# Performance work log

Hardware: AMD Instinct MI355X
Metric: run time of the kernel (lower is better)

## Reference

```python
import jax, jax.numpy as jnp
import numpy as np

HEADS = 8
DIM_HEAD = 64

def setup_inputs() -> dict:
    key = jax.random.key(0)
    ks = jax.random.split(key, 9)
    B, N1, N2, D = 4, 2048, 2048, 1024
    inner = HEADS * DIM_HEAD  # 512
    s_in = 1.0 / np.sqrt(D)
    s_inner = 1.0 / np.sqrt(inner)
    return {
        "x1": jax.random.normal(ks[0], (B, N1, D), jnp.float32),
        "x2": jax.random.normal(ks[1], (B, N2, D), jnp.float32),
        "Wq1": jax.random.normal(ks[2], (D, inner), jnp.float32) * s_in,
        "Wk1": jax.random.normal(ks[3], (D, inner), jnp.float32) * s_in,
        "Wv1": jax.random.normal(ks[4], (D, inner), jnp.float32) * s_in,
        "Wk2": jax.random.normal(ks[5], (D, inner), jnp.float32) * s_in,
        "Wv2": jax.random.normal(ks[6], (D, inner), jnp.float32) * s_in,
        "Wo": jax.random.normal(ks[7], (inner, D), jnp.float32) * s_inner,
        "bo": jnp.zeros((D,), jnp.float32),
    }

def reference(x1, x2, Wq1, Wk1, Wv1, Wk2, Wv2, Wo, bo):
    h, d = HEADS, DIM_HEAD
    scale = d ** (-0.5)
    B, N1, _ = x1.shape
    N2 = x2.shape[1]

    def split_heads(t, n):
        return t.reshape(B, n, h, d)  # [B, n, h, d]

    q1 = split_heads(x1 @ Wq1, N1)
    k1 = split_heads(x1 @ Wk1, N1)
    v1 = split_heads(x1 @ Wv1, N1)
    k2 = split_heads(x2 @ Wk2, N2)
    v2 = split_heads(x2 @ Wv2, N2)

    k = jnp.concatenate([k1, k2], axis=1)  # [B, N1+N2, h, d]
    v = jnp.concatenate([v1, v2], axis=1)

    # fp32 precision for QK^T (matches _ATTN_PRECISION == 'fp32')
    sim = jnp.einsum('bihd,bjhd->bhij', q1.astype(jnp.float32),
                     k.astype(jnp.float32)) * scale  # [B, h, N1, N1+N2]
    attn = jax.nn.softmax(sim, axis=-1)
    out = jnp.einsum('bhij,bjhd->bihd', attn, v)  # [B, N1, h, d]
    out = out.reshape(B, N1, h * d)
    return out @ Wo + bo
```

## Files before the change

kernel.cpp:

```cpp
#include <hip/hip_runtime.h>
#include <stdint.h>

typedef __bf16 bf16x8 __attribute__((ext_vector_type(8)));
typedef float f32x4 __attribute__((ext_vector_type(4)));
typedef unsigned short ushort_t;

#define MFMA16(a,b,c) __builtin_amdgcn_mfma_f32_16x16x32_bf16((a),(b),(c),0,0,0)

__device__ __forceinline__ unsigned short f2bf(float f){
    unsigned u = __builtin_bit_cast(unsigned, f);
    u += 0x7fffu + ((u>>16)&1u);
    return (unsigned short)(u>>16);
}
__device__ __forceinline__ unsigned pack2bf(float lo, float hi){
    unsigned a = __builtin_bit_cast(unsigned, lo) + 0x8000u;
    unsigned b = __builtin_bit_cast(unsigned, hi) + 0x8000u;
    return __builtin_amdgcn_perm(b, a, 0x07060302u);
}
__device__ __forceinline__ float fexp2(float x){
#if __has_builtin(__builtin_amdgcn_exp2f)
    return __builtin_amdgcn_exp2f(x);
#else
    return exp2f(x);
#endif
}

__device__ __forceinline__ void async16(ushort_t* lds, const ushort_t* g){
#if __has_builtin(__builtin_amdgcn_global_load_lds)
    __builtin_amdgcn_global_load_lds(
        (const __attribute__((address_space(1))) void*)g,
        (__attribute__((address_space(3))) void*)lds, 16, 0, 0);
#else
    const int l = (int)(threadIdx.x & 63u);
    *(uint4*)(lds + (size_t)l*8) = *(const uint4*)g;
#endif
}

__global__ __launch_bounds__(256) void convert_x(const float* __restrict__ src,
                                                 ushort_t* __restrict__ dst){
    size_t i = ((size_t)blockIdx.x*256 + threadIdx.x)*8;
    float4 a = *(const float4*)(src + i);
    float4 b = *(const float4*)(src + i + 4);
    uint4 o;
    o.x = pack2bf(a.x, a.y); o.y = pack2bf(a.z, a.w);
    o.z = pack2bf(b.x, b.y); o.w = pack2bf(b.z, b.w);
    *(uint4*)(dst + i) = o;
}

__global__ __launch_bounds__(256) void transpose_w(
    const float* __restrict__ w0, const float* __restrict__ w1,
    const float* __restrict__ w2, const float* __restrict__ w3,
    const float* __restrict__ w4,
    ushort_t* __restrict__ Wt1, ushort_t* __restrict__ Wt2)
{
    int z = blockIdx.z;
    const float* src; ushort_t* dst;
    if (z < 3)  { src = (z==0)?w0:((z==1)?w1:w2); dst = Wt1 + (size_t)z*512*1024; }
    else        { src = (z==3)?w3:w4;             dst = Wt2 + (size_t)(z-3)*512*1024; }
    const int K = 1024, N = 512;
    int k0 = blockIdx.x*32, n0 = blockIdx.y*32;
    __shared__ float T[32][33];
    int t = threadIdx.x;
    int kr = t>>3, nc = (t&7)*4;
    float4 v = *(const float4*)(src + (size_t)(k0+kr)*N + n0 + nc);
    T[kr][nc] = v.x; T[kr][nc+1] = v.y; T[kr][nc+2] = v.z; T[kr][nc+3] = v.w;
    __syncthreads();
    int nr = t>>3, kc = (t&7)*4;
    uint2 o;
    o.x = pack2bf(T[kc][nr],   T[kc+1][nr]);
    o.y = pack2bf(T[kc+2][nr], T[kc+3][nr]);
    *(uint2*)(dst + (size_t)(n0+nr)*K + k0 + kc) = o;
    (void)K;
}

__global__ __launch_bounds__(256) void transpose_wo(
    const float* __restrict__ src, ushort_t* __restrict__ dst)
{
    __shared__ float T[64][33];
    const int k0 = blockIdx.x*64;
    const int n0 = blockIdx.y*32;
    const int t = threadIdx.x;
    const int kr = t>>3, nc = (t&7)*4;
#pragma unroll
    for (int hf = 0; hf < 2; ++hf){
        float4 v = *(const float4*)(src + (size_t)(k0 + hf*32 + kr)*1024 + n0 + nc);
        T[hf*32+kr][nc]   = v.x; T[hf*32+kr][nc+1] = v.y;
        T[hf*32+kr][nc+2] = v.z; T[hf*32+kr][nc+3] = v.w;
    }
    __syncthreads();
    const int nr = t>>3, kc = (t&7)*8;
    ushort_t tmp[8];
#pragma unroll
    for (int e = 0; e < 8; ++e){
        int dp = kc + e;
        int d  = ((dp&3)<<4) | (dp>>2);
        tmp[e] = f2bf(T[d][nr]);
    }
    *(uint4*)(dst + (size_t)(n0+nr)*512 + k0 + kc) = *(uint4*)tmp;
}

template<int KD, int MODE>
__global__ __launch_bounds__(256) void gemm_bt(
    const ushort_t* __restrict__ A, const ushort_t* __restrict__ Bt,
    ushort_t* __restrict__ Qp, ushort_t* __restrict__ Kp, ushort_t* __restrict__ Vtp,
    float* __restrict__ outF, const float* __restrict__ bias, int koff)
{
    __shared__ ushort_t As[2][128][32];
    __shared__ ushort_t Bs[2][128][32];
    const int t = threadIdx.x;
    const int m0 = blockIdx.x*128, n0 = blockIdx.y*128;
    const int w = t>>6, l = t&63;
    const int quad = l>>4, lc = l&15;
    const int wr = (w>>1)*64, wc = (w&1)*64;

    f32x4 acc[4][4] = {};

    const int crow = l>>2;
    const int kseg = (l&3)*8;
    const ushort_t* gA0 = A  + (size_t)(m0 + w*32      + crow)*KD + kseg;
    const ushort_t* gA1 = A  + (size_t)(m0 + w*32 + 16 + crow)*KD + kseg;
    const ushort_t* gB0 = Bt + (size_t)(n0 + w*32      + crow)*KD + kseg;
    const ushort_t* gB1 = Bt + (size_t)(n0 + w*32 + 16 + crow)*KD + kseg;

    const int NK = KD/32;

    async16(&As[0][w*32][0],    gA0);
    async16(&As[0][w*32+16][0], gA1);
    async16(&Bs[0][w*32][0],    gB0);
    async16(&Bs[0][w*32+16][0], gB1);
    __syncthreads();

    for (int kk = 0; kk < NK; ++kk) {
        const int cur = kk & 1;
        if (kk + 1 < NK) {
            const int k0 = (kk+1)*32;
            const int nx = cur ^ 1;
            async16(&As[nx][w*32][0],    gA0 + k0);
            async16(&As[nx][w*32+16][0], gA1 + k0);
            async16(&Bs[nx][w*32][0],    gB0 + k0);
            async16(&Bs[nx][w*32+16][0], gB1 + k0);
        }
        bf16x8 af[4], bfv[4];
#pragma unroll
        for (int i = 0; i < 4; ++i) {
            af[i]  = *(const bf16x8*)&As[cur][wr + i*16 + lc][quad*8];
            bfv[i] = *(const bf16x8*)&Bs[cur][wc + i*16 + lc][quad*8];
        }
#pragma unroll
        for (int mt = 0; mt < 4; ++mt)
#pragma unroll
            for (int nt = 0; nt < 4; ++nt)
                acc[mt][nt] = MFMA16(af[mt], bfv[nt], acc[mt][nt]);
        __syncthreads();
    }

    if (MODE == 2) {
        float bv[4];
#pragma unroll
        for (int nt = 0; nt < 4; ++nt) bv[nt] = bias[n0 + wc + nt*16 + lc];
#pragma unroll
        for (int mt = 0; mt < 4; ++mt) {
            const int row = m0 + wr + mt*16 + quad*4;
#pragma unroll
            for (int nt = 0; nt < 4; ++nt) {
                const int col = n0 + wc + nt*16 + lc;
#pragma unroll
                for (int r = 0; r < 4; ++r)
                    outF[(size_t)(row+r)*1024 + col] = acc[mt][nt][r] + bv[nt];
            }
        }
    } else {
        const int sub = (MODE == 0) ? (n0>>9) : (1 + (n0>>9));
        const int hh  = ((n0 + wc)>>6) & 7;
        const int dp  = 4*lc;
        const float QSC = 0.18033688011112042f;
        if (sub == 0) {
#pragma unroll
            for (int mt = 0; mt < 4; ++mt) {
                const int row = m0 + wr + mt*16 + quad*4;
                const int b = row>>11, i = row & 2047;
#pragma unroll
                for (int r = 0; r < 4; ++r) {
                    uint2 o;
                    o.x = pack2bf(acc[mt][0][r]*QSC, acc[mt][1][r]*QSC);
                    o.y = pack2bf(acc[mt][2][r]*QSC, acc[mt][3][r]*QSC);
                    *(uint2*)(Qp + ((size_t)(b*8+hh)*2048 + i + r)*64 + dp) = o;
                }
            }
        } else if (sub == 1) {
#pragma unroll
            for (int mt = 0; mt < 4; ++mt) {
                const int row = m0 + wr + mt*16 + quad*4;
                const int b = row>>11, i = row & 2047;
#pragma unroll
                for (int r = 0; r < 4; ++r) {
                    uint2 o;
                    o.x = pack2bf(acc[mt][0][r], acc[mt][1][r]);
                    o.y = pack2bf(acc[mt][2][r], acc[mt][3][r]);
                    *(uint2*)(Kp + ((size_t)(b*8+hh)*4096 + koff + i + r)*64 + dp) = o;
                }
            }
        } else {
#pragma unroll
            for (int mt = 0; mt < 4; ++mt) {
                const int row = m0 + wr + mt*16 + quad*4;
                const int b = row>>11, i = row & 2047;
#pragma unroll
                for (int nt = 0; nt < 4; ++nt) {
                    uint2 o;
                    o.x = pack2bf(acc[mt][nt][0], acc[mt][nt][1]);
                    o.y = pack2bf(acc[mt][nt][2], acc[mt][nt][3]);
                    *(uint2*)(Vtp + ((size_t)(b*8+hh)*64 + dp + nt)*4096 + koff + i) = o;
                }
            }
        }
    }
}

__global__ __launch_bounds__(256) void flash_attn(
    const ushort_t* __restrict__ Q, const ushort_t* __restrict__ Kg,
    const ushort_t* __restrict__ Vt, ushort_t* __restrict__ AO)
{
    __shared__ ushort_t Ks[2][64][72];
    __shared__ ushort_t Vs[2][64][72];
    const int bh = blockIdx.x, qt = blockIdx.y;
    const int b = bh>>3, h = bh&7;
    const int t = threadIdx.x, wv = t>>6, l = t&63;
    const int quad = l>>4, lc = l&15;

    const ushort_t* qbase = Q + ((size_t)bh*2048 + qt*128 + wv*16 + lc)*64;
    bf16x8 qA0 = *(const bf16x8*)(qbase + quad*8);
    bf16x8 qA1 = *(const bf16x8*)(qbase + 32 + quad*8);
    bf16x8 qB0 = *(const bf16x8*)(qbase + 64*64 + quad*8);
    bf16x8 qB1 = *(const bf16x8*)(qbase + 64*64 + 32 + quad*8);

    const ushort_t* Kb = Kg + (size_t)bh*4096*64;
    const ushort_t* Vb = Vt + (size_t)bh*64*4096;

    const int srow   = t>>2;
    const int schunk = t&3;
    const ushort_t* kst = Kb + (size_t)srow*64   + schunk*16;
    const ushort_t* vst = Vb + (size_t)srow*4096 + schunk*16;
    const int vcol = (schunk>>1)*32 + (schunk&1)*4;

    float l0 = 0.0f, l1 = 0.0f;
    f32x4 o0[4] = {}, o1[4] = {};

    uint4 ka  = *(const uint4*)(kst);
    uint4 kb2 = *(const uint4*)(kst + 8);
    uint4 va  = *(const uint4*)(vst);
    uint4 vb2 = *(const uint4*)(vst + 8);

    for (int jt = 0; jt < 64; ++jt) {
        const int cur = jt & 1;
        ushort_t* ksd = &Ks[cur][srow][schunk*16];
        ushort_t* vsd = &Vs[cur][srow][vcol];
        *(uint4*)ksd     = ka;
        *(uint4*)(ksd+8) = kb2;
        { uint2 t0; t0.x = va.x;  t0.y = va.y;  *(uint2*)(vsd)      = t0; }
        { uint2 t1; t1.x = va.z;  t1.y = va.w;  *(uint2*)(vsd + 8)  = t1; }
        { uint2 t2; t2.x = vb2.x; t2.y = vb2.y; *(uint2*)(vsd + 16) = t2; }
        { uint2 t3; t3.x = vb2.z; t3.y = vb2.w; *(uint2*)(vsd + 24) = t3; }
        __syncthreads();
        if (jt < 63) {
            const int j0 = (jt+1)*64;
            ka  = *(const uint4*)(kst + (size_t)j0*64);
            kb2 = *(const uint4*)(kst + (size_t)j0*64 + 8);
            va  = *(const uint4*)(vst + j0);
            vb2 = *(const uint4*)(vst + j0 + 8);
        }

        f32x4 s0[4], s1[4];
#pragma unroll
        for (int kt = 0; kt < 4; ++kt) {
            bf16x8 kf0 = *(const bf16x8*)&Ks[cur][kt*16 + lc][quad*8];
            bf16x8 kf1 = *(const bf16x8*)&Ks[cur][kt*16 + lc][32 + quad*8];
            f32x4 z0 = {}, z1 = {};
            z0 = MFMA16(kf0, qA0, z0); z0 = MFMA16(kf1, qA1, z0);
            z1 = MFMA16(kf0, qB0, z1); z1 = MFMA16(kf1, qB1, z1);
            s0[kt] = z0; s1[kt] = z1;
        }

        union { unsigned u[8]; bf16x8 v[2]; } p0, p1;
        float rs0 = 0.0f, rs1 = 0.0f;
#pragma unroll
        for (int kt = 0; kt < 4; ++kt) {
            float a0 = fexp2(s0[kt][0]), a1v = fexp2(s0[kt][1]);
            float a2 = fexp2(s0[kt][2]), a3 = fexp2(s0[kt][3]);
            rs0 += (a0 + a1v) + (a2 + a3);
            p0.u[kt*2]   = pack2bf(a0, a1v);
            p0.u[kt*2+1] = pack2bf(a2, a3);
            float c0 = fexp2(s1[kt][0]), c1 = fexp2(s1[kt][1]);
            float c2 = fexp2(s1[kt][2]), c3 = fexp2(s1[kt][3]);
            rs1 += (c0 + c1) + (c2 + c3);
            p1.u[kt*2]   = pack2bf(c0, c1);
            p1.u[kt*2+1] = pack2bf(c2, c3);
        }
        l0 += rs0; l1 += rs1;

#pragma unroll
        for (int dt = 0; dt < 4; ++dt) {
            bf16x8 vf0 = *(const bf16x8*)&Vs[cur][dt*16 + lc][quad*8];
            bf16x8 vf1 = *(const bf16x8*)&Vs[cur][dt*16 + lc][32 + quad*8];
            o0[dt] = MFMA16(vf0, p0.v[0], o0[dt]);
            o0[dt] = MFMA16(vf1, p0.v[1], o0[dt]);
            o1[dt] = MFMA16(vf0, p1.v[0], o1[dt]);
            o1[dt] = MFMA16(vf1, p1.v[1], o1[dt]);
        }
    }

    l0 += __shfl_xor(l0, 16); l0 += __shfl_xor(l0, 32);
    l1 += __shfl_xor(l1, 16); l1 += __shfl_xor(l1, 32);
    float li0 = 1.0f / l0, li1 = 1.0f / l1;

    const int qA = qt*128 + wv*16 + lc;
    ushort_t* aodA = AO + ((size_t)b*2048 + qA)*512 + h*64 + quad*4;
    ushort_t* aodB = aodA + (size_t)64*512;
#pragma unroll
    for (int dt = 0; dt < 4; ++dt) {
        uint2 oa, ob;
        oa.x = pack2bf(o0[dt][0]*li0, o0[dt][1]*li0);
        oa.y = pack2bf(o0[dt][2]*li0, o0[dt][3]*li0);
        *(uint2*)(aodA + dt*16) = oa;
        ob.x = pack2bf(o1[dt][0]*li1, o1[dt][1]*li1);
        ob.y = pack2bf(o1[dt][2]*li1, o1[dt][3]*li1);
        *(uint2*)(aodB + dt*16) = ob;
    }
}

extern "C" void kernel_launch(void* const* d_in, const int* in_sizes, int n_in,
                              void* d_out, int out_size, void* d_ws, size_t ws_size,
                              hipStream_t stream)
{
    const float* x1  = (const float*)d_in[0];
    const float* x2  = (const float*)d_in[1];
    const float* Wq1 = (const float*)d_in[2];
    const float* Wk1 = (const float*)d_in[3];
    const float* Wv1 = (const float*)d_in[4];
    const float* Wk2 = (const float*)d_in[5];
    const float* Wv2 = (const float*)d_in[6];
    const float* Wo  = (const float*)d_in[7];
    const float* bo  = (const float*)d_in[8];
    float* out = (float*)d_out;

    ushort_t* ws  = (ushort_t*)d_ws;
    ushort_t* Xc1 = ws;
    ushort_t* Xc2 = Xc1 + 8388608;
    ushort_t* Wt1 = Xc2 + 8388608;
    ushort_t* Wt2 = Wt1 + 1572864;
    ushort_t* Wot = Wt2 + 1048576;
    ushort_t* Qp  = Wot + 524288;
    ushort_t* Kp  = Qp  + 4194304;
    ushort_t* Vtp = Kp  + 8388608;
    ushort_t* AOp = Xc2;

    convert_x<<<4096, 256, 0, stream>>>(x1, Xc1);
    convert_x<<<4096, 256, 0, stream>>>(x2, Xc2);
    transpose_w<<<dim3(32,16,5), 256, 0, stream>>>(Wq1,Wk1,Wv1,Wk2,Wv2, Wt1,Wt2);
    transpose_wo<<<dim3(8,32), 256, 0, stream>>>(Wo, Wot);

    gemm_bt<1024,0><<<dim3(64,12), 256, 0, stream>>>(Xc1, Wt1, Qp, Kp, Vtp, nullptr, nullptr, 0);
    gemm_bt<1024,1><<<dim3(64,8),  256, 0, stream>>>(Xc2, Wt2, Qp, Kp, Vtp, nullptr, nullptr, 2048);

    flash_attn<<<dim3(32,16), 256, 0, stream>>>(Qp, Kp, Vtp, AOp);

    gemm_bt<512,2><<<dim3(64,8), 256, 0, stream>>>(AOp, Wot, nullptr, nullptr, nullptr, out, bo, 0);
}
```

Before: 303.6 us.

## Split attention KV range across two blocks and merge partials in a combine kernel

Templates the flash attention kernel on a KV split factor and launches two blocks per (batch-head, query tile), each covering half of the key/value sequence. Each half writes unnormalized fp32 output partials and row sums to workspace, and a new combine kernel adds them, normalizes, and writes bf16 attention output. The aim is to double the number of blocks, improving CU occupancy and latency hiding on a grid that otherwise only has 512 blocks. In exchange it adds an extra kernel launch and fp32 partial traffic through global memory. It runs only if the workspace is large enough, otherwise it falls back to the single-pass kernel.

```diff
diff --git a/kernel.cpp b/kernel.cpp
--- a/kernel.cpp
+++ b/kernel.cpp
@@ -217,13 +217,18 @@
     }
 }
 
-__global__ __launch_bounds__(256) void flash_attn(
+template<int SPLIT>
+__global__ __launch_bounds__(256) void flash_attn_k(
     const ushort_t* __restrict__ Q, const ushort_t* __restrict__ Kg,
-    const ushort_t* __restrict__ Vt, ushort_t* __restrict__ AO)
-{
+    const ushort_t* __restrict__ Vt, ushort_t* __restrict__ AO,
+    float* __restrict__ P0, float* __restrict__ P1, float* __restrict__ Lp)
+{
+    constexpr int NJT = 64 / SPLIT;
     __shared__ ushort_t Ks[2][64][72];
     __shared__ ushort_t Vs[2][64][72];
     const int bh = blockIdx.x, qt = blockIdx.y;
+    const int sp = (SPLIT > 1) ? (int)blockIdx.z : 0;
+    const int jt0 = sp * NJT;
     const int b = bh>>3, h = bh&7;
     const int t = threadIdx.x, wv = t>>6, l = t&63;
     const int quad = l>>4, lc = l&15;
@@ -246,12 +251,13 @@
     float l0 = 0.0f, l1 = 0.0f;
     f32x4 o0[4] = {}, o1[4] = {};
 
-    uint4 ka  = *(const uint4*)(kst);
-    uint4 kb2 = *(const uint4*)(kst + 8);
-    uint4 va  = *(const uint4*)(vst);
-    uint4 vb2 = *(const uint4*)(vst + 8);
-
-    for (int jt = 0; jt < 64; ++jt) {
+    const size_t kq0 = (size_t)jt0*64;
+    uint4 ka  = *(const uint4*)(kst + kq0*64);
+    uint4 kb2 = *(const uint4*)(kst + kq0*64 + 8);
+    uint4 va  = *(const uint4*)(vst + kq0);
+    uint4 vb2 = *(const uint4*)(vst + kq0 + 8);
+
+    for (int jt = 0; jt < NJT; ++jt) {
         const int cur = jt & 1;
         ushort_t* ksd = &Ks[cur][srow][schunk*16];
         ushort_t* vsd = &Vs[cur][srow][vcol];
@@ -262,10 +268,10 @@
         { uint2 t2; t2.x = vb2.x; t2.y = vb2.y; *(uint2*)(vsd + 16) = t2; }
         { uint2 t3; t3.x = vb2.z; t3.y = vb2.w; *(uint2*)(vsd + 24) = t3; }
         __syncthreads();
-        if (jt < 63) {
-            const int j0 = (jt+1)*64;
-            ka  = *(const uint4*)(kst + (size_t)j0*64);
-            kb2 = *(const uint4*)(kst + (size_t)j0*64 + 8);
+        if (jt < NJT - 1) {
+            const size_t j0 = (size_t)(jt0 + jt + 1)*64;
+            ka  = *(const uint4*)(kst + j0*64);
+            kb2 = *(const uint4*)(kst + j0*64 + 8);
             va  = *(const uint4*)(vst + j0);
             vb2 = *(const uint4*)(vst + j0 + 8);
         }
@@ -311,20 +317,63 @@
 
     l0 += __shfl_xor(l0, 16); l0 += __shfl_xor(l0, 32);
     l1 += __shfl_xor(l1, 16); l1 += __shfl_xor(l1, 32);
-    float li0 = 1.0f / l0, li1 = 1.0f / l1;
-
-    const int qA = qt*128 + wv*16 + lc;
-    ushort_t* aodA = AO + ((size_t)b*2048 + qA)*512 + h*64 + quad*4;
-    ushort_t* aodB = aodA + (size_t)64*512;
-#pragma unroll
-    for (int dt = 0; dt < 4; ++dt) {
-        uint2 oa, ob;
-        oa.x = pack2bf(o0[dt][0]*li0, o0[dt][1]*li0);
-        oa.y = pack2bf(o0[dt][2]*li0, o0[dt][3]*li0);
-        *(uint2*)(aodA + dt*16) = oa;
-        ob.x = pack2bf(o1[dt][0]*li1, o1[dt][1]*li1);
-        ob.y = pack2bf(o1[dt][2]*li1, o1[dt][3]*li1);
-        *(uint2*)(aodB + dt*16) = ob;
+
+    if (SPLIT == 1) {
+        float li0 = 1.0f / l0, li1 = 1.0f / l1;
+        const int qA = qt*128 + wv*16 + lc;
+        ushort_t* aodA = AO + ((size_t)b*2048 + qA)*512 + h*64 + quad*4;
+        ushort_t* aodB = aodA + (size_t)64*512;
+#pragma unroll
+        for (int dt = 0; dt < 4; ++dt) {
+            uint2 oa, ob;
+            oa.x = pack2bf(o0[dt][0]*li0, o0[dt][1]*li0);
+            oa.y = pack2bf(o0[dt][2]*li0, o0[dt][3]*li0);
+            *(uint2*)(aodA + dt*16) = oa;
+            ob.x = pack2bf(o1[dt][0]*li1, o1[dt][1]*li1);
+            ob.y = pack2bf(o1[dt][2]*li1, o1[dt][3]*li1);
+            *(uint2*)(aodB + dt*16) = ob;
+        }
+    } else {
+        float* P = sp ? P1 : P0;
+        const int bid = bh*16 + qt;
+        const int qrA = wv*16 + lc;
+        const size_t pbA = ((size_t)bid*128 + qrA)*64;
+        const size_t pbB = pbA + (size_t)64*64;
+#pragma unroll
+        for (int dt = 0; dt < 4; ++dt) {
+            *(f32x4*)(P + pbA + dt*16 + quad*4) = o0[dt];
+            *(f32x4*)(P + pbB + dt*16 + quad*4) = o1[dt];
+        }
+        if (l < 16) {
+            Lp[((size_t)sp*512 + bid)*128 + qrA]      = l0;
+            Lp[((size_t)sp*512 + bid)*128 + 64 + qrA] = l1;
+        }
+    }
+}
+
+__global__ __launch_bounds__(256) void combine_attn(
+    const float* __restrict__ P0, const float* __restrict__ P1,
+    const float* __restrict__ Lp, ushort_t* __restrict__ AO)
+{
+    const int bid = blockIdx.x;
+    const int bh = bid>>4, qt = bid&15;
+    const int b = bh>>3, h = bh&7;
+    const int t = threadIdx.x;
+    const int dcol = (t&15)*4;
+    const size_t pblk = (size_t)bid*8192;
+#pragma unroll
+    for (int e = 0; e < 8; ++e) {
+        const int qrow = e*16 + (t>>4);
+        const size_t idx = pblk + (size_t)qrow*64 + dcol;
+        float4 a = *(const float4*)(P0 + idx);
+        float4 c = *(const float4*)(P1 + idx);
+        float ls = Lp[(size_t)bid*128 + qrow] + Lp[(size_t)(512 + bid)*128 + qrow];
+        float inv = 1.0f / ls;
+        uint2 o;
+        o.x = pack2bf((a.x + c.x)*inv, (a.y + c.y)*inv);
+        o.y = pack2bf((a.z + c.z)*inv, (a.w + c.w)*inv);
+        ushort_t* ao = AO + ((size_t)b*2048 + qt*128 + qrow)*512 + h*64 + dcol;
+        *(uint2*)ao = o;
     }
 }
 
@@ -352,6 +401,8 @@
     ushort_t* Qp  = Wot + 524288;
     ushort_t* Kp  = Qp  + 4194304;
     ushort_t* Vtp = Kp  + 8388608;
+    ushort_t* Pex = Vtp + 8388608;
+    ushort_t* Lex = Pex + 8388608;
     ushort_t* AOp = Xc2;
 
     convert_x<<<4096, 256, 0, stream>>>(x1, Xc1);
@@ -362,7 +413,16 @@
     gemm_bt<1024,0><<<dim3(64,12), 256, 0, stream>>>(Xc1, Wt1, Qp, Kp, Vtp, nullptr, nullptr, 0);
     gemm_bt<1024,1><<<dim3(64,8),  256, 0, stream>>>(Xc2, Wt2, Qp, Kp, Vtp, nullptr, nullptr, 2048);
 
-    flash_attn<<<dim3(32,16), 256, 0, stream>>>(Qp, Kp, Vtp, AOp);
+    const size_t NEED = 99090432ull;
+    if (ws_size >= NEED) {
+        float* P0f = (float*)Xc1;
+        float* P1f = (float*)Pex;
+        float* Lf  = (float*)Lex;
+        flash_attn_k<2><<<dim3(32,16,2), 256, 0, stream>>>(Qp, Kp, Vtp, nullptr, P0f, P1f, Lf);
+        combine_attn<<<512, 256, 0, stream>>>(P0f, P1f, Lf, AOp);
+    } else {
+        flash_attn_k<1><<<dim3(32,16,1), 256, 0, stream>>>(Qp, Kp, Vtp, AOp, nullptr, nullptr, nullptr);
+    }
 
     gemm_bt<512,2><<<dim3(64,8), 256, 0, stream>>>(AOp, Wot, nullptr, nullptr, nullptr, out, bo, 0);
 }
```

After: 307.2 us. No clear change (+1.2%).
